# Optimization experiments

Measured on AMD Instinct MI355X. Metric: run time of the kernel, lower is better.

## Reference

```python
import jax, jax.numpy as jnp
import numpy as np

B, C, D, H, W = 1, 32, 48, 64, 208
EPS = 1e-5  # BatchNorm eps


def setup_inputs() -> dict:
    key = jax.random.key(0)
    ks = jax.random.split(key, 8)
    x = jax.random.normal(ks[0], (B, C, D, H, W), jnp.float32)
    g = jax.random.normal(ks[1], (B, 20, H, W), jnp.float32)
    conv_w = jax.random.normal(ks[2], (C, C, 3, 3, 3), jnp.float32) * 0.02
    bn1_gamma = 1.0 + 0.1 * jax.random.normal(ks[3], (C,), jnp.float32)
    bn1_beta = 0.1 * jax.random.normal(ks[4], (C,), jnp.float32)
    bn1_mean = 0.1 * jax.random.normal(ks[5], (C,), jnp.float32)
    bn1_var = jax.random.uniform(ks[6], (C,), jnp.float32, 0.5, 1.5)
    bn2_gamma = 1.0 + 0.1 * jax.random.normal(ks[7], (C,), jnp.float32)
    bn2_beta = jnp.zeros((C,), jnp.float32)
    bn2_mean = jnp.zeros((C,), jnp.float32)
    bn2_var = jnp.ones((C,), jnp.float32)
    return {
        'x': x, 'g': g, 'conv_w': conv_w,
        'bn1_gamma': bn1_gamma, 'bn1_beta': bn1_beta, 'bn1_mean': bn1_mean, 'bn1_var': bn1_var,
        'bn2_gamma': bn2_gamma, 'bn2_beta': bn2_beta, 'bn2_mean': bn2_mean, 'bn2_var': bn2_var,
    }


def _l1_normalize(k):
    # F.normalize(k, p=1, dim=1)
    return k / jnp.maximum(jnp.sum(jnp.abs(k), axis=1, keepdims=True), 1e-12)


def _sga_scan(x, w):
    """Directional semi-global aggregation along the LAST axis.
    x: [B,C,D,H,L] cost volume, w: [B,5,H,L] L1-normalized guidance weights.
    Recurrence (GANet SGA):
      A[p,d] = w0*x[p,d] + w1*A[p-1,d] + w2*A[p-1,d-1] + w3*A[p-1,d+1] + w4*max_d' A[p-1,d']
    """
    xs = jnp.moveaxis(x, -1, 0)  # [L,B,C,D,H]
    ws = jnp.moveaxis(w, -1, 0)  # [L,B,5,H]

    def step(prev, inp):
        xi, wi = inp  # [B,C,D,H], [B,5,H]
        w0, w1, w2, w3, w4 = [wi[:, i][:, None, None, :] for i in range(5)]
        up = jnp.concatenate([prev[:, :, :1], prev[:, :, :-1]], axis=2)   # A[d-1]
        dn = jnp.concatenate([prev[:, :, 1:], prev[:, :, -1:]], axis=2)   # A[d+1]
        mx = jnp.max(prev, axis=2, keepdims=True)                          # max_d A
        out = w0 * xi + w1 * prev + w2 * up + w3 * dn + w4 * mx
        return out, out

    _, outs = jax.lax.scan(step, xs[0], (xs, ws))  # boundary: carry init = raw cost slice
    return jnp.moveaxis(outs, 0, -1)


def _sga(x, k1, k2, k3, k4):
    # direction 1: left -> right (along W)
    d1 = _sga_scan(x, k1)
    # direction 2: right -> left
    d2 = jnp.flip(_sga_scan(jnp.flip(x, -1), jnp.flip(k2, -1)), -1)
    # vertical directions: swap H<->W so the scan axis is H
    xv = jnp.swapaxes(x, 3, 4)  # [B,C,D,W,H]
    d3 = jnp.swapaxes(_sga_scan(xv, jnp.swapaxes(k3, 2, 3)), 3, 4)  # top -> bottom
    d4 = jnp.swapaxes(
        jnp.flip(_sga_scan(jnp.flip(xv, -1), jnp.flip(jnp.swapaxes(k4, 2, 3), -1)), -1), 3, 4)
    # GANet combines directions with an elementwise max
    return jnp.maximum(jnp.maximum(d1, d2), jnp.maximum(d3, d4))


def _bn3d(x, gamma, beta, mean, var):
    s = (gamma / jnp.sqrt(var + EPS))[None, :, None, None, None]
    return (x - mean[None, :, None, None, None]) * s + beta[None, :, None, None, None]


def _conv3d_same(x, w):
    return jax.lax.conv_general_dilated(
        x, w, window_strides=(1, 1, 1), padding=[(1, 1)] * 3,
        dimension_numbers=('NCDHW', 'OIDHW', 'NCDHW'))


def reference(x, g, conv_w, bn1_gamma, bn1_beta, bn1_mean, bn1_var,
              bn2_gamma, bn2_beta, bn2_mean, bn2_var):
    rem = x
    k1, k2, k3, k4 = jnp.split(g, 4, axis=1)  # each [B,5,H,W]
    k1, k2, k3, k4 = map(_l1_normalize, (k1, k2, k3, k4))
    a = _sga(x, k1, k2, k3, k4)
    # refine=True branch: BN+ReLU then BasicConv(3x3x3, BN, no relu)
    a = jax.nn.relu(_bn3d(a, bn1_gamma, bn1_beta, bn1_mean, bn1_var))
    a = _conv3d_same(a, conv_w)
    a = _bn3d(a, bn2_gamma, bn2_beta, bn2_mean, bn2_var)
    return jax.nn.relu(a + rem)
```

## Files before the change

### kernel.cpp

```cpp
#include <hip/hip_runtime.h>
#include <hip/hip_bf16.h>
#include <cstddef>

#define C_ 32
#define D_ 48
#define DP_ 50
#define H_ 64
#define W_ 208
#define WP_ 210
#define HW_ 13312
#define HS_ 9984
#define EPS_ 1e-5f

typedef __attribute__((ext_vector_type(8))) short short8;
typedef __attribute__((ext_vector_type(4))) float float4v;
typedef __attribute__((ext_vector_type(16))) float float16v;
typedef __attribute__((ext_vector_type(2))) __fp16 half2v;

template<int CTRL>
__device__ __forceinline__ float dppmov(float x) {
    int v = __builtin_bit_cast(int, x);
    return __builtin_bit_cast(float,
        __builtin_amdgcn_update_dpp(v, v, CTRL, 0xf, 0xf, false));
}
template<int CTRL>
__device__ __forceinline__ float dppmax(float m) {
    return fmaxf(m, dppmov<CTRL>(m));
}
__device__ __forceinline__ float rl(float v, int idx) {
    return __builtin_bit_cast(float,
        __builtin_amdgcn_readlane(__builtin_bit_cast(int, v), idx));
}

__device__ __forceinline__ float sga_step_dpp(float A, float xi,
    float w0, float w1, float w2, float w3, float w4, bool actv, bool ge47)
{
    float up = dppmov<0x138>(A);
    float dn = dppmov<0x130>(A);
    dn = ge47 ? A : dn;
    float m = actv ? A : -3.4e38f;
    m = dppmax<0x111>(m);
    m = dppmax<0x112>(m);
    m = dppmax<0x114>(m);
    m = dppmax<0x118>(m);
    m = dppmax<0x142>(m);
    m = dppmax<0x143>(m);
    float mall = rl(m, 63);
    return (w0*xi + w1*A) + ((w2*up + w3*dn) + w4*mall);
}

__global__ __launch_bounds__(256) void prep_kernel(
    const float* __restrict__ g, const float* __restrict__ cw,
    float* __restrict__ wn, float* __restrict__ wnT,
    __hip_bfloat16* __restrict__ wrep, unsigned* __restrict__ actu)
{
    int idx = blockIdx.x * 256 + threadIdx.x;
    if (idx < 4 * HW_) {
        int dir = idx / HW_;
        int hw  = idx % HW_;
        const float* gb = g + dir * 5 * HW_ + hw;
        float v0 = gb[0*HW_], v1 = gb[1*HW_], v2 = gb[2*HW_], v3 = gb[3*HW_], v4 = gb[4*HW_];
        float s = fabsf(v0)+fabsf(v1)+fabsf(v2)+fabsf(v3)+fabsf(v4);
        float inv = 1.0f / fmaxf(s, 1e-12f);
        v0 *= inv; v1 *= inv; v2 *= inv; v3 *= inv; v4 *= inv;
        float* ob = wn + dir * 5 * HW_ + hw;
        ob[0*HW_] = v0; ob[1*HW_] = v1; ob[2*HW_] = v2; ob[3*HW_] = v3; ob[4*HW_] = v4;
        if (dir >= 2) {
            int hq = hw / W_, wq = hw % W_;
            float* oT = wnT + ((size_t)((dir-2)*5)*W_ + wq)*H_ + hq;
            oT[0]       = v0; oT[1*HW_] = v1; oT[2*HW_] = v2;
            oT[3*HW_]   = v3; oT[4*HW_] = v4;
        }
    } else if (idx < 4 * HW_ + 27648) {
        int j = idx - 4 * HW_;
        int e    = j & 7;
        int lane = (j >> 3) & 63;
        int q    = j >> 9;
        int cih  = q & 1;
        int tap  = q >> 1;
        int co = lane & 31;
        int ci = cih * 16 + (lane >> 5) * 8 + e;
        wrep[j] = __float2bfloat16(cw[(co * C_ + ci) * 27 + tap]);
    } else if (idx < 4 * HW_ + 27648 + 98304) {
        int j2 = idx - (4 * HW_ + 27648);
        int hd  = j2 >> 5;
        int r   = j2 & 31;
        int col = (r >> 4) ? 209 : 0;
        int cu  = r & 15;
        int h = hd / 48, dd = hd % 48;
        actu[(((size_t)h * DP_ + dd + 1) * WP_ + col) * 16 + cu] = 0u;
    } else {
        int j3 = idx - (4 * HW_ + 27648 + 98304);
        int pl   = j3 >= 215040;
        int r3   = pl ? j3 - 215040 : j3;
        int h    = r3 / 3360;
        int rest = r3 % 3360;
        int dpad = pl ? (DP_ - 1) : 0;
        actu[((size_t)h * DP_ + dpad) * WP_ * 16 + rest] = 0u;
    }
}

__global__ __launch_bounds__(256) void t0_kernel(
    const float* __restrict__ x, __hip_bfloat16* __restrict__ xt)
{
    __shared__ float t[48 * 257];
    int tid = threadIdx.x;
    int c  = blockIdx.x / 52;
    int q0 = (blockIdx.x % 52) * 256;
    #pragma unroll
    for (int dd = 0; dd < 48; ++dd)
        t[dd * 257 + tid] = x[((size_t)c * 48 + dd) * HW_ + q0 + tid];
    __syncthreads();
    unsigned* xtu = (unsigned*)xt;
    #pragma unroll
    for (int k = 0; k < 24; ++k) {
        int f = tid + 256 * k;
        int d2 = f % 24, hwl = f / 24;
        union { unsigned u; __hip_bfloat16 hh[2]; } pk;
        pk.hh[0] = __float2bfloat16(t[(2 * d2) * 257 + hwl]);
        pk.hh[1] = __float2bfloat16(t[(2 * d2 + 1) * 257 + hwl]);
        xtu[(((size_t)c * HW_ + q0 + hwl) * 48 + 2 * d2) >> 1] = pk.u;
    }
}

template<int LN>
__device__ __forceinline__ float chunk_fwd(float A,
    const __hip_bfloat16* __restrict__ xp, __hip_bfloat16* __restrict__ dp,
    const float* __restrict__ wb, int P0, int lane, bool actv, bool ge47)
{
    float xr[LN];
    #pragma unroll
    for (int j = 0; j < LN; ++j) xr[j] = __bfloat162float(xp[(size_t)(P0 + j) * 48]);
    int lm = lane & (LN - 1);
    float wv0 = wb[0*HW_ + P0 + lm], wv1 = wb[1*HW_ + P0 + lm],
          wv2 = wb[2*HW_ + P0 + lm], wv3 = wb[3*HW_ + P0 + lm],
          wv4 = wb[4*HW_ + P0 + lm];
    #pragma unroll
    for (int j = 0; j < LN; ++j) {
        A = sga_step_dpp(A, xr[j], rl(wv0,j), rl(wv1,j), rl(wv2,j),
                         rl(wv3,j), rl(wv4,j), actv, ge47);
        if (actv) dp[(size_t)(P0 + j) * 48] = __float2bfloat16(A);
    }
    return A;
}

template<int LN>
__device__ __forceinline__ float chunk_rev(float A,
    const __hip_bfloat16* __restrict__ xp, __hip_bfloat16* __restrict__ dp,
    const float* __restrict__ wb, int P0, int lane, bool actv, bool ge47)
{
    float xr[LN]; __hip_bfloat16 dr[LN];
    #pragma unroll
    for (int j = 0; j < LN; ++j) {
        xr[j] = __bfloat162float(xp[(size_t)(P0 + j) * 48]);
        dr[j] = dp[(size_t)(P0 + j) * 48];
    }
    int lm = lane & (LN - 1);
    float wv0 = wb[0*HW_ + P0 + lm], wv1 = wb[1*HW_ + P0 + lm],
          wv2 = wb[2*HW_ + P0 + lm], wv3 = wb[3*HW_ + P0 + lm],
          wv4 = wb[4*HW_ + P0 + lm];
    #pragma unroll
    for (int j = LN - 1; j >= 0; --j) {
        A = sga_step_dpp(A, xr[j], rl(wv0,j), rl(wv1,j), rl(wv2,j),
                         rl(wv3,j), rl(wv4,j), actv, ge47);
        if (actv)
            dp[(size_t)(P0 + j) * 48] =
                __float2bfloat16(fmaxf(__bfloat162float(dr[j]), A));
    }
    return A;
}

__global__ __launch_bounds__(256) void sga_w_kernel(
    const __hip_bfloat16* __restrict__ xt, const float* __restrict__ wn,
    __hip_bfloat16* __restrict__ d12)
{
    int lane = threadIdx.x & 63;
    int wid  = blockIdx.x * 4 + (threadIdx.x >> 6);
    int c = wid >> 6, h = wid & 63;
    int d = lane < 48 ? lane : 47;
    bool actv = lane < 48, ge47 = lane >= 47;
    const __hip_bfloat16* xp = xt + ((size_t)c * HW_ + h * W_) * 48 + d;
    __hip_bfloat16* dp = d12 + ((size_t)c * HW_ + h * W_) * 48 + d;
    const float* w1 = wn + (size_t)0 * 5 * HW_ + h * W_;
    const float* w2 = wn + (size_t)1 * 5 * HW_ + h * W_;

    float A = __bfloat162float(xp[0]);
    for (int cc = 0; cc < 6; ++cc)
        A = chunk_fwd<32>(A, xp, dp, w1, cc * 32, lane, actv, ge47);
    A = chunk_fwd<16>(A, xp, dp, w1, 192, lane, actv, ge47);

    A = __bfloat162float(xp[(size_t)207 * 48]);
    A = chunk_rev<16>(A, xp, dp, w2, 192, lane, actv, ge47);
    for (int cc = 0; cc < 6; ++cc)
        A = chunk_rev<32>(A, xp, dp, w2, 160 - cc * 32, lane, actv, ge47);
}

__global__ __launch_bounds__(256, 6) void sga_h_kernel(
    const __hip_bfloat16* __restrict__ xt, const float* __restrict__ wnT,
    __hip_bfloat16* __restrict__ d12,
    const float* __restrict__ g1, const float* __restrict__ b1,
    const float* __restrict__ m1, const float* __restrict__ v1)
{
    __shared__ __fp16 sA[2][2][64][48];

    int lane = threadIdx.x & 63;
    int widb = threadIdx.x >> 6;
    int colb = widb >> 1;
    int dir  = widb & 1;
    int gcol = blockIdx.x * 2 + colb;
    int c = gcol / W_, w = gcol % W_;
    int d = lane < 48 ? lane : 47;
    bool actv = lane < 48, ge47 = lane >= 47;
    const __hip_bfloat16* xp = xt + ((size_t)c * HW_ + w) * 48 + d;
    const float* wb = wnT + ((size_t)(dir * 5) * W_ + w) * H_;
    int il = lane >> 3, jl = lane & 7;
    bool wact = il < 5;

    float xb[3][8];
    float wAr[3];

    if (dir == 0) {
        #pragma unroll
        for (int j = 0; j < 8; ++j) {
            xb[0][j] = __bfloat162float(xp[(size_t)j * HS_]);
            xb[1][j] = __bfloat162float(xp[(size_t)(8 + j) * HS_]);
        }
        wAr[0] = wact ? wb[il * HW_ + jl] : 0.0f;
        wAr[1] = wact ? wb[il * HW_ + 8 + jl] : 0.0f;
        float A = xb[0][0];
        #pragma unroll
        for (int cc = 0; cc < 8; ++cc) {
            const int buf = cc % 3;
            if (cc < 6) {
                const int nb = (cc + 2) % 3;
                #pragma unroll
                for (int j = 0; j < 8; ++j)
                    xb[nb][j] = __bfloat162float(xp[(size_t)((cc + 2) * 8 + j) * HS_]);
                wAr[nb] = wact ? wb[il * HW_ + (cc + 2) * 8 + jl] : 0.0f;
            }
            #pragma unroll
            for (int j = 0; j < 8; ++j) {
                A = sga_step_dpp(A, xb[buf][j], rl(wAr[buf], j), rl(wAr[buf], 8 + j),
                                 rl(wAr[buf], 16 + j), rl(wAr[buf], 24 + j),
                                 rl(wAr[buf], 32 + j), actv, ge47);
                if (actv) sA[colb][0][cc * 8 + j][d] = (__fp16)A;
            }
        }
    } else {
        #pragma unroll
        for (int j = 0; j < 8; ++j) {
            xb[0][j] = __bfloat162float(xp[(size_t)(56 + j) * HS_]);
            xb[1][j] = __bfloat162float(xp[(size_t)(48 + j) * HS_]);
        }
        wAr[0] = wact ? wb[il * HW_ + 56 + jl] : 0.0f;
        wAr[1] = wact ? wb[il * HW_ + 48 + jl] : 0.0f;
        float A = xb[0][7];
        #pragma unroll
        for (int cc2 = 0; cc2 < 8; ++cc2) {
            const int cc = 7 - cc2;
            const int buf = cc2 % 3;
            if (cc2 < 6) {
                const int nb = (cc2 + 2) % 3;
                #pragma unroll
                for (int j = 0; j < 8; ++j)
                    xb[nb][j] = __bfloat162float(xp[(size_t)((cc - 2) * 8 + j) * HS_]);
                wAr[nb] = wact ? wb[il * HW_ + (cc - 2) * 8 + jl] : 0.0f;
            }
            #pragma unroll
            for (int j = 7; j >= 0; --j) {
                A = sga_step_dpp(A, xb[buf][j], rl(wAr[buf], j), rl(wAr[buf], 8 + j),
                                 rl(wAr[buf], 16 + j), rl(wAr[buf], 24 + j),
                                 rl(wAr[buf], 32 + j), actv, ge47);
                if (actv) sA[colb][1][cc * 8 + j][d] = (__fp16)A;
            }
        }
    }

    __syncthreads();

    float s1 = g1[c] * rsqrtf(v1[c] + EPS_);
    float o1 = b1[c] - m1[c] * s1;
    __hip_bfloat16* dp = d12 + ((size_t)c * HW_ + w) * 48 + d;
    #pragma unroll
    for (int t = 0; t < 32; ++t) {
        int h = dir * 32 + t;
        float dv = __bfloat162float(dp[(size_t)h * HS_]);
        float d3 = (float)sA[colb][0][h][d];
        float d4 = (float)sA[colb][1][h][d];
        float comb = fmaxf(fmaxf(d3, d4), dv);
        if (actv)
            dp[(size_t)h * HS_] = __float2bfloat16(fmaxf(comb * s1 + o1, 0.0f));
    }
}

__global__ __launch_bounds__(256) void trans_kernel(
    const __hip_bfloat16* __restrict__ st, __hip_bfloat16* __restrict__ act)
{
    __shared__ float t[8 * 1571];
    int tid = threadIdx.x;
    int h  = blockIdx.x / 26;
    int w0 = (blockIdx.x % 26) * 8;
    const unsigned* stu = (const unsigned*)st;
    #pragma unroll
    for (int k = 0; k < 24; ++k) {
        int f = tid + 256 * k;
        int d2 = f % 24, wl = (f / 24) % 8, c = f / 192;
        unsigned u = stu[(((size_t)c * HW_ + h * W_ + w0 + wl) * 48 + 2 * d2) >> 1];
        const __hip_bfloat16* bp = (const __hip_bfloat16*)&u;
        t[wl * 1571 + c * 49 + 2 * d2]     = __bfloat162float(bp[0]);
        t[wl * 1571 + c * 49 + 2 * d2 + 1] = __bfloat162float(bp[1]);
    }
    __syncthreads();
    unsigned* actu = (unsigned*)act;
    #pragma unroll
    for (int k = 0; k < 24; ++k) {
        int f = tid + 256 * k;
        int cp = f % 16, wl = (f / 16) % 8, d = f / 128;
        union { unsigned u; __hip_bfloat16 hh[2]; } pk;
        pk.hh[0] = __float2bfloat16(t[wl * 1571 + (2 * cp) * 49 + d]);
        pk.hh[1] = __float2bfloat16(t[wl * 1571 + (2 * cp + 1) * 49 + d]);
        actu[(((size_t)h * DP_ + d + 1) * WP_ + w0 + wl + 1) * 16 + cp] = pk.u;
    }
}

__global__ __launch_bounds__(256, 4) void conv_kernel(
    const __hip_bfloat16* __restrict__ act,
    const short8* __restrict__ wrep,
    const float* __restrict__ x,
    const float* __restrict__ g2, const float* __restrict__ b2,
    const float* __restrict__ m2, const float* __restrict__ v2,
    float* __restrict__ out)
{
    __shared__ __hip_bfloat16 sAct[10 * 34 * 40];

    int tid  = threadIdx.x;
    int lane = tid & 63;
    int v    = tid >> 6;
    int bid  = blockIdx.x;
    int wt   = bid % 7;
    int t    = bid / 7;
    int h    = t & 63;
    int d0b  = (t >> 6) * 8;
    int w0   = wt * 32;
    int n    = lane & 31;
    int half = lane >> 5;

    float16v acc0 = (float16v)(0.0f);
    float16v acc1 = (float16v)(0.0f);

    const short8* ap8 = (const short8*)act;

    #pragma unroll
    for (int kh = 0; kh < 3; ++kh) {
        int hh = h + kh - 1;
        if (hh < 0 || hh >= H_) continue;
        __syncthreads();
        #pragma unroll
        for (int k = 0; k < 6; ++k) {
            int i = tid + 256 * k;
            if (i < 1360) {
                int dp = i / 136;
                int r  = i - dp * 136;
                int wl = r >> 2, q = r & 3;
                int wc = w0 + wl; wc = wc < 209 ? wc : 209;
                short8 vd = ap8[(((size_t)hh * DP_ + d0b + dp) * WP_ + wc) * 4 + q];
                *(short8*)&sAct[(dp * 34 + wl) * 40 + q * 8] = vd;
            }
        }
        __syncthreads();
        #pragma unroll
        for (int kw = 0; kw < 3; ++kw) {
            #pragma unroll
            for (int cih = 0; cih < 2; ++cih) {
                short8 af[3];
                #pragma unroll
                for (int kd = 0; kd < 3; ++kd)
                    af[kd] = wrep[(((kd*3 + kh)*3 + kw)*2 + cih)*64 + lane];
                short8 bf[4];
                #pragma unroll
                for (int p = 0; p < 4; ++p)
                    bf[p] = *(const short8*)
                        &sAct[((2*v + p) * 34 + kw + n) * 40 + cih * 16 + half * 8];
                #pragma unroll
                for (int kd = 0; kd < 3; ++kd) {
                    acc0 = __builtin_amdgcn_mfma_f32_32x32x16_bf16(af[kd], bf[kd],   acc0, 0, 0, 0);
                    acc1 = __builtin_amdgcn_mfma_f32_32x32x16_bf16(af[kd], bf[kd+1], acc1, 0, 0, 0);
                }
            }
        }
    }

    int d0 = d0b + 2 * v;
    int wl = w0 + n;
    bool wvalid = wl < W_;
    int coh = 4 * half;
    #pragma unroll
    for (int r = 0; r < 16; ++r) {
        int co = (r & 3) + 8 * (r >> 2) + coh;
        float s2 = g2[co] * rsqrtf(v2[co] + EPS_);
        float o2 = b2[co] - m2[co] * s2;
        size_t idx0 = ((size_t)(co * D_ + d0) * H_ + h) * W_ + wl;
        if (wvalid) {
            out[idx0]       = fmaxf(acc0[r] * s2 + o2 + x[idx0],       0.0f);
            out[idx0 + HW_] = fmaxf(acc1[r] * s2 + o2 + x[idx0 + HW_], 0.0f);
        }
    }
}

extern "C" void kernel_launch(void* const* d_in, const int* in_sizes, int n_in,
                              void* d_out, int out_size, void* d_ws, size_t ws_size,
                              hipStream_t stream)
{
    const float* x    = (const float*)d_in[0];
    const float* g    = (const float*)d_in[1];
    const float* cw   = (const float*)d_in[2];
    const float* bn1g = (const float*)d_in[3];
    const float* bn1b = (const float*)d_in[4];
    const float* bn1m = (const float*)d_in[5];
    const float* bn1v = (const float*)d_in[6];
    const float* bn2g = (const float*)d_in[7];
    const float* bn2b = (const float*)d_in[8];
    const float* bn2m = (const float*)d_in[9];
    const float* bn2v = (const float*)d_in[10];
    float* out = (float*)d_out;

    char* ws = (char*)d_ws;
    float* wn  = (float*)ws;
    float* wnT = (float*)(ws + 1064960);
    __hip_bfloat16* wrep = (__hip_bfloat16*)(ws + 1597440);
    __hip_bfloat16* d12t = (__hip_bfloat16*)(ws + 1652736);
    __hip_bfloat16* act  = (__hip_bfloat16*)(ws + 42547200);
    __hip_bfloat16* xt = (__hip_bfloat16*)out;

    prep_kernel<<<2380, 256, 0, stream>>>(g, cw, wn, wnT, wrep, (unsigned*)act);
    t0_kernel<<<1664, 256, 0, stream>>>(x, xt);
    sga_w_kernel<<<512, 256, 0, stream>>>(xt, wn, d12t);
    sga_h_kernel<<<3328, 256, 0, stream>>>(xt, wnT, d12t, bn1g, bn1b, bn1m, bn1v);
    trans_kernel<<<1664, 256, 0, stream>>>(d12t, act);
    conv_kernel<<<2688, 256, 0, stream>>>(act, (const short8*)wrep, x,
                                          bn2g, bn2b, bn2m, bn2v, out);
}
```

Before: 415.7 us.

## Run forward and reverse W-direction SGA scans concurrently in separate wavefronts

The W-direction aggregation kernel now gives each (c,h) row a 128-thread block with two wavefronts, one scanning forward and one scanning in reverse, instead of one wavefront running both scans back to back. Each wave keeps its own half of the outputs packed as fp16 in registers and hands the other half to its partner through shared memory, then writes the max of both directions once. This removes the serial dependency between the two scans and the read-modify-write of the intermediate buffer. The loop also adds a triple-buffered prefetch of x and guidance weights in 8-step chunks. The cost is a large register array (52 packed values plus the prefetch buffers), fp16 rounding of intermediates before the bf16 store, and a block-wide barrier.

```diff
diff --git a/kernel.cpp b/kernel.cpp
--- a/kernel.cpp
+++ b/kernel.cpp
@@ -123,76 +123,129 @@
     }
 }
 
-template<int LN>
-__device__ __forceinline__ float chunk_fwd(float A,
-    const __hip_bfloat16* __restrict__ xp, __hip_bfloat16* __restrict__ dp,
-    const float* __restrict__ wb, int P0, int lane, bool actv, bool ge47)
-{
-    float xr[LN];
-    #pragma unroll
-    for (int j = 0; j < LN; ++j) xr[j] = __bfloat162float(xp[(size_t)(P0 + j) * 48]);
-    int lm = lane & (LN - 1);
-    float wv0 = wb[0*HW_ + P0 + lm], wv1 = wb[1*HW_ + P0 + lm],
-          wv2 = wb[2*HW_ + P0 + lm], wv3 = wb[3*HW_ + P0 + lm],
-          wv4 = wb[4*HW_ + P0 + lm];
-    #pragma unroll
-    for (int j = 0; j < LN; ++j) {
-        A = sga_step_dpp(A, xr[j], rl(wv0,j), rl(wv1,j), rl(wv2,j),
-                         rl(wv3,j), rl(wv4,j), actv, ge47);
-        if (actv) dp[(size_t)(P0 + j) * 48] = __float2bfloat16(A);
-    }
-    return A;
-}
-
-template<int LN>
-__device__ __forceinline__ float chunk_rev(float A,
-    const __hip_bfloat16* __restrict__ xp, __hip_bfloat16* __restrict__ dp,
-    const float* __restrict__ wb, int P0, int lane, bool actv, bool ge47)
-{
-    float xr[LN]; __hip_bfloat16 dr[LN];
-    #pragma unroll
-    for (int j = 0; j < LN; ++j) {
-        xr[j] = __bfloat162float(xp[(size_t)(P0 + j) * 48]);
-        dr[j] = dp[(size_t)(P0 + j) * 48];
-    }
-    int lm = lane & (LN - 1);
-    float wv0 = wb[0*HW_ + P0 + lm], wv1 = wb[1*HW_ + P0 + lm],
-          wv2 = wb[2*HW_ + P0 + lm], wv3 = wb[3*HW_ + P0 + lm],
-          wv4 = wb[4*HW_ + P0 + lm];
-    #pragma unroll
-    for (int j = LN - 1; j >= 0; --j) {
-        A = sga_step_dpp(A, xr[j], rl(wv0,j), rl(wv1,j), rl(wv2,j),
-                         rl(wv3,j), rl(wv4,j), actv, ge47);
-        if (actv)
-            dp[(size_t)(P0 + j) * 48] =
-                __float2bfloat16(fmaxf(__bfloat162float(dr[j]), A));
-    }
-    return A;
-}
-
-__global__ __launch_bounds__(256) void sga_w_kernel(
+__global__ __launch_bounds__(128, 4) void sga_w_kernel(
     const __hip_bfloat16* __restrict__ xt, const float* __restrict__ wn,
     __hip_bfloat16* __restrict__ d12)
 {
+    __shared__ __fp16 sO[2][104][48];
+
     int lane = threadIdx.x & 63;
-    int wid  = blockIdx.x * 4 + (threadIdx.x >> 6);
+    int dir  = threadIdx.x >> 6;
+    int wid  = blockIdx.x;
     int c = wid >> 6, h = wid & 63;
     int d = lane < 48 ? lane : 47;
     bool actv = lane < 48, ge47 = lane >= 47;
     const __hip_bfloat16* xp = xt + ((size_t)c * HW_ + h * W_) * 48 + d;
+    const float* wb = wn + (size_t)dir * 5 * HW_ + h * W_;
+    int il = lane >> 3, jl = lane & 7;
+    bool wact = il < 5;
+
+    unsigned selfp[52];
+    float xb[3][8];
+    float wAr[3];
+
+    if (dir == 0) {
+        #pragma unroll
+        for (int j = 0; j < 8; ++j) {
+            xb[0][j] = __bfloat162float(xp[(size_t)j * 48]);
+            xb[1][j] = __bfloat162float(xp[(size_t)(8 + j) * 48]);
+        }
+        wAr[0] = wact ? wb[il * HW_ + jl] : 0.0f;
+        wAr[1] = wact ? wb[il * HW_ + 8 + jl] : 0.0f;
+        float A = xb[0][0];
+        float Aev = 0.0f;
+        #pragma unroll
+        for (int cc = 0; cc < 26; ++cc) {
+            const int buf = cc % 3;
+            if (cc < 24) {
+                const int nb = (cc + 2) % 3;
+                #pragma unroll
+                for (int j = 0; j < 8; ++j)
+                    xb[nb][j] = __bfloat162float(xp[(size_t)((cc + 2) * 8 + j) * 48]);
+                wAr[nb] = wact ? wb[il * HW_ + (cc + 2) * 8 + jl] : 0.0f;
+            }
+            #pragma unroll
+            for (int j = 0; j < 8; ++j) {
+                A = sga_step_dpp(A, xb[buf][j], rl(wAr[buf], j), rl(wAr[buf], 8 + j),
+                                 rl(wAr[buf], 16 + j), rl(wAr[buf], 24 + j),
+                                 rl(wAr[buf], 32 + j), actv, ge47);
+                const int p = cc * 8 + j;
+                if (p < 104) {
+                    if (j & 1) {
+                        half2v pk2 = __builtin_amdgcn_cvt_pkrtz(Aev, A);
+                        selfp[p >> 1] = __builtin_bit_cast(unsigned, pk2);
+                    } else {
+                        Aev = A;
+                    }
+                } else {
+                    if (actv) sO[0][p - 104][d] = (__fp16)A;
+                }
+            }
+        }
+    } else {
+        #pragma unroll
+        for (int j = 0; j < 8; ++j) {
+            xb[0][j] = __bfloat162float(xp[(size_t)(200 + j) * 48]);
+            xb[1][j] = __bfloat162float(xp[(size_t)(192 + j) * 48]);
+        }
+        wAr[0] = wact ? wb[il * HW_ + 200 + jl] : 0.0f;
+        wAr[1] = wact ? wb[il * HW_ + 192 + jl] : 0.0f;
+        float A = xb[0][7];
+        float Aod = 0.0f;
+        #pragma unroll
+        for (int cc2 = 0; cc2 < 26; ++cc2) {
+            const int cc = 25 - cc2;
+            const int buf = cc2 % 3;
+            if (cc2 < 24) {
+                const int nb = (cc2 + 2) % 3;
+                #pragma unroll
+                for (int j = 0; j < 8; ++j)
+                    xb[nb][j] = __bfloat162float(xp[(size_t)((cc - 2) * 8 + j) * 48]);
+                wAr[nb] = wact ? wb[il * HW_ + (cc - 2) * 8 + jl] : 0.0f;
+            }
+            #pragma unroll
+            for (int j = 7; j >= 0; --j) {
+                A = sga_step_dpp(A, xb[buf][j], rl(wAr[buf], j), rl(wAr[buf], 8 + j),
+                                 rl(wAr[buf], 16 + j), rl(wAr[buf], 24 + j),
+                                 rl(wAr[buf], 32 + j), actv, ge47);
+                const int p = cc * 8 + j;
+                if (p >= 104) {
+                    const int q = p - 104;
+                    if (j & 1) {
+                        Aod = A;
+                    } else {
+                        half2v pk2 = __builtin_amdgcn_cvt_pkrtz(A, Aod);
+                        selfp[q >> 1] = __builtin_bit_cast(unsigned, pk2);
+                    }
+                } else {
+                    if (actv) sO[1][p][d] = (__fp16)A;
+                }
+            }
+        }
+    }
+
+    __syncthreads();
+
     __hip_bfloat16* dp = d12 + ((size_t)c * HW_ + h * W_) * 48 + d;
-    const float* w1 = wn + (size_t)0 * 5 * HW_ + h * W_;
-    const float* w2 = wn + (size_t)1 * 5 * HW_ + h * W_;
-
-    float A = __bfloat162float(xp[0]);
-    for (int cc = 0; cc < 6; ++cc)
-        A = chunk_fwd<32>(A, xp, dp, w1, cc * 32, lane, actv, ge47);
-    A = chunk_fwd<16>(A, xp, dp, w1, 192, lane, actv, ge47);
-
-    A = __bfloat162float(xp[(size_t)207 * 48]);
-    A = chunk_rev<16>(A, xp, dp, w2, 192, lane, actv, ge47);
-    for (int cc = 0; cc < 6; ++cc)
-        A = chunk_rev<32>(A, xp, dp, w2, 160 - cc * 32, lane, actv, ge47);
+    if (actv) {
+        if (dir == 0) {
+            #pragma unroll
+            for (int p = 0; p < 104; ++p) {
+                half2v hp = __builtin_bit_cast(half2v, selfp[p >> 1]);
+                float mine = (float)((p & 1) ? hp[1] : hp[0]);
+                float oth  = (float)sO[1][p][d];
+                dp[(size_t)p * 48] = __float2bfloat16(fmaxf(mine, oth));
+            }
+        } else {
+            #pragma unroll
+            for (int q = 0; q < 104; ++q) {
+                half2v hp = __builtin_bit_cast(half2v, selfp[q >> 1]);
+                float mine = (float)((q & 1) ? hp[1] : hp[0]);
+                float oth  = (float)sO[0][q][d];
+                dp[(size_t)(104 + q) * 48] = __float2bfloat16(fmaxf(mine, oth));
+            }
+        }
+    }
 }
 
 __global__ __launch_bounds__(256, 6) void sga_h_kernel(
@@ -434,7 +487,7 @@
 
     prep_kernel<<<2380, 256, 0, stream>>>(g, cw, wn, wnT, wrep, (unsigned*)act);
     t0_kernel<<<1664, 256, 0, stream>>>(x, xt);
-    sga_w_kernel<<<512, 256, 0, stream>>>(xt, wn, d12t);
+    sga_w_kernel<<<2048, 128, 0, stream>>>(xt, wn, d12t);
     sga_h_kernel<<<3328, 256, 0, stream>>>(xt, wnT, d12t, bn1g, bn1b, bn1m, bn1v);
     trans_kernel<<<1664, 256, 0, stream>>>(d12t, act);
     conv_kernel<<<2688, 256, 0, stream>>>(act, (const short8*)wrep, x,
```

New measurement: 504.7 us. +21.4%, slower.
